# Kernel tuning notes

Hardware: AMD Instinct MI355X
Metric: run time of the kernel (lower is better)

The kernel has to match this reference:

```python
import jax, jax.numpy as jnp
import numpy as np

BATCH = 1048576
INPUT_DIM = 64
DEPTH = 7
N_INTERNAL = 2 ** DEPTH - 1  # 127
N_LEAVES = 2 ** DEPTH        # 128


def setup_inputs() -> dict:
    key = jax.random.key(0)
    kx, kw = jax.random.split(key)
    x = jax.random.normal(kx, (BATCH, INPUT_DIM), dtype=jnp.float32)
    node_weights = jax.random.normal(kw, (N_INTERNAL, INPUT_DIM), dtype=jnp.float32) * 0.01
    node_biases = jnp.zeros((N_INTERNAL,), dtype=jnp.float32)
    leaf_values = jnp.linspace(0.0, 1.0, N_LEAVES, dtype=jnp.float32)
    return {"x": x, "node_weights": node_weights, "node_biases": node_biases,
            "leaf_values": leaf_values}


def _leaf_probs(x, node_weights, node_biases, depth):
    # All node routing probabilities in one GEMM (BFS node order matches idx order).
    logits = jnp.einsum('bd,nd->bn', x, node_weights) + node_biases  # [B, n_internal]
    p_right = jax.nn.sigmoid(logits)
    batch = x.shape[0]
    probs = jnp.ones((batch, 1), dtype=x.dtype)  # root prob
    idx = 0
    for d in range(depth):
        n = 1 << d
        pd = p_right[:, idx:idx + n]  # [B, n] nodes at level d in BFS order
        # child order: left (2*node) then right (2*node+1) -> interleave
        probs = jnp.stack([probs * (1.0 - pd), probs * pd], axis=-1).reshape(batch, 2 * n)
        idx += n
    return probs  # [B, n_leaves]


def reference(x, node_weights, node_biases, leaf_values):
    leaf_probs = _leaf_probs(x, node_weights, node_biases, DEPTH)
    pred = leaf_probs @ leaf_values  # [B]
    return (pred, leaf_probs)
```

## Files before the change

kernel.cpp:

```cpp
#include <hip/hip_runtime.h>


typedef float v4f __attribute__((ext_vector_type(4)));
typedef _Float16 h8 __attribute__((ext_vector_type(8)));
typedef unsigned int u32;
typedef u32 u32x2 __attribute__((ext_vector_type(2)));

constexpr int BATCH = 1 << 20;
constexpr int PSTRIDE = 40;
constexpr int PWAVE = 128 * PSTRIDE;

__device__ __forceinline__ float fast_sigmoid(float z) {
    float e = __builtin_amdgcn_exp2f(z * -1.44269504088896340736f);
    return __builtin_amdgcn_rcpf(1.0f + e);
}

__device__ __forceinline__ u32 pk2(float a, float b) {
    return __builtin_bit_cast(u32, __builtin_amdgcn_cvt_pkrtz(a, b));
}

__device__ __forceinline__ h8 cvt8(v4f lo, v4f hi) {
    union { u32 w[4]; h8 v; } u;
    u.w[0] = pk2(lo.x, lo.y);
    u.w[1] = pk2(lo.z, lo.w);
    u.w[2] = pk2(hi.x, hi.y);
    u.w[3] = pk2(hi.z, hi.w);
    return u.v;
}

__global__ __launch_bounds__(256, 3) void sdt_kernel(
    const float* __restrict__ x,
    const float* __restrict__ w,
    const float* __restrict__ bias,
    const float* __restrict__ leaf,
    float* __restrict__ pred_out,
    float* __restrict__ lp_out)
{
    __shared__ __align__(16) unsigned char smem[4 * PWAVE];

    const int tid  = threadIdx.x;
    const int lane = tid & 63;
    const int wave = tid >> 6;
    const int lc = lane & 15, lq = lane >> 4;
    const int j = lane & 7,   rsub = lane >> 3;

    unsigned char* Pw = smem + wave * PWAVE;

    h8 bfrag[8][2];
#pragma unroll
    for (int ct = 0; ct < 8; ++ct) {
        int node = ct * 16 + lc; if (node > 126) node = 126;
#pragma unroll
        for (int kh = 0; kh < 2; ++kh) {
            const float* src = w + node * 64 + kh * 32 + lq * 8;
            bfrag[ct][kh] = cvt8(*(const v4f*)src, *(const v4f*)(src + 4));
        }
    }
    float bias_v[8];
#pragma unroll
    for (int ct = 0; ct < 8; ++ct) {
        int node = ct * 16 + lc; if (node > 126) node = 126;
        bias_v[ct] = bias[node];
    }
    v4f leafv[4];
#pragma unroll
    for (int s = 0; s < 4; ++s) leafv[s] = *(const v4f*)(leaf + 32 * s + 4 * j);

    const int b2 = (j >> 2) & 1, b3 = (j >> 1) & 1, b4 = j & 1;
    const int wave_row0 = blockIdx.x * 256 + wave * 16;

    const float* xr0 = x + (size_t)(wave_row0 + lc) * 64 + lq * 8;
    v4f xa = *(const v4f*)xr0,        xb = *(const v4f*)(xr0 + 4);
    v4f xc = *(const v4f*)(xr0 + 32), xd = *(const v4f*)(xr0 + 36);

#pragma unroll
    for (int ck = 0; ck < 4; ++ck) {
        const int row0 = wave_row0 + ck * 64;

        h8 a0 = cvt8(xa, xb);
        h8 a1 = cvt8(xc, xd);
        if (ck < 3) {
            const float* xr = xr0 + (ck + 1) * 64 * 64;
            xa = *(const v4f*)xr;        xb = *(const v4f*)(xr + 4);
            xc = *(const v4f*)(xr + 32); xd = *(const v4f*)(xr + 36);
        }

#pragma unroll
        for (int ct = 0; ct < 8; ++ct) {
            v4f acc = {};
            acc = __builtin_amdgcn_mfma_f32_16x16x32_f16(a0, bfrag[ct][0], acc, 0, 0, 0);
            acc = __builtin_amdgcn_mfma_f32_16x16x32_f16(a1, bfrag[ct][1], acc, 0, 0, 0);
            float s0 = fast_sigmoid(acc[0] + bias_v[ct]);
            float s1 = fast_sigmoid(acc[1] + bias_v[ct]);
            float s2 = fast_sigmoid(acc[2] + bias_v[ct]);
            float s3 = fast_sigmoid(acc[3] + bias_v[ct]);
            *(u32x2*)(Pw + (ct * 16 + lc) * PSTRIDE + lq * 8) =
                u32x2{pk2(s0, s1), pk2(s2, s3)};
        }

        asm volatile("s_waitcnt lgkmcnt(0)" ::: "memory");

        auto rd = [&](int node, int row) -> float {
            return (float)*(const _Float16*)(Pw + node * PSTRIDE + row * 2);
        };

        float pa = 0.f, pb = 0.f;
#pragma unroll
        for (int i1 = 0; i1 < 2; ++i1) {
            const int row = rsub + 8 * i1;
            float p0  = rd(0, row);
            float p1a = rd(1, row), p1b = rd(2, row);
            float f01_0 = (1.f - p0) * (1.f - p1a);
            float f01_1 = (1.f - p0) * p1a;
            float f01_2 = p0 * (1.f - p1b);
            float f01_3 = p0 * p1b;
            float acc = 0.f;
            v4f* dst = (v4f*)lp_out + (size_t)(row0 + row) * 32 + j;
#pragma unroll
            for (int seg = 0; seg < 4; ++seg) {
                float f01 = seg == 0 ? f01_0 : seg == 1 ? f01_1 : seg == 2 ? f01_2 : f01_3;
                float pd2 = rd(3 + seg, row);
                float P3 = f01 * (b2 ? pd2 : 1.f - pd2);
                float pd3 = rd(7 + 2 * seg + (j >> 2), row);
                float P4 = P3 * (b3 ? pd3 : 1.f - pd3);
                float pd4 = rd(15 + 4 * seg + (j >> 1), row);
                float P5 = P4 * (b4 ? pd4 : 1.f - pd4);
                const int q = 8 * seg + j;
                float pd5 = rd(31 + q, row);
                float A = P5 * (1.f - pd5), B = P5 * pd5;
                float pl = rd(63 + 2 * q, row), pr = rd(64 + 2 * q, row);
                v4f o = { A * (1.f - pl), A * pl, B * (1.f - pr), B * pr };
                dst[seg * 8] = o;
                acc = fmaf(o.x, leafv[seg].x, acc);
                acc = fmaf(o.y, leafv[seg].y, acc);
                acc = fmaf(o.z, leafv[seg].z, acc);
                acc = fmaf(o.w, leafv[seg].w, acc);
            }
            if (i1 == 0) pa = acc; else pb = acc;
        }

#pragma unroll
        for (int s = 1; s <= 4; s <<= 1) {
            pa += __shfl_xor(pa, s, 64);
            pb += __shfl_xor(pb, s, 64);
        }
        if (j == 0) {
            pred_out[row0 + rsub]     = pa;
            pred_out[row0 + rsub + 8] = pb;
        }
    }
}

extern "C" void kernel_launch(void* const* d_in, const int* in_sizes, int n_in,
                              void* d_out, int out_size, void* d_ws, size_t ws_size,
                              hipStream_t stream) {
    const float* x    = (const float*)d_in[0];
    const float* w    = (const float*)d_in[1];
    const float* bias = (const float*)d_in[2];
    const float* leaf = (const float*)d_in[3];

    float* pred = (float*)d_out;
    float* lp   = (float*)d_out + BATCH;

    sdt_kernel<<<BATCH / 256, 256, 0, stream>>>(x, w, bias, leaf, pred, lp);
}
```

Before: 178.7 us.

## Stage node weights in swizzled LDS and raise occupancy to four blocks

Node weights are no longer kept as per-lane register fragments. They are converted once per block into an XOR-swizzled fp16 tile in shared memory, and the B fragments are read from LDS inside the GEMM loop. This frees registers so launch bounds can target four blocks per CU, which should help hide the latency of the heavy lp_out stores. The branchy left/right selects are replaced with fma using precomputed sign and offset constants. The cost is extra LDS traffic, 16KB more shared memory per block, and a block-wide sync.

```diff
diff --git a/kernel.cpp b/kernel.cpp
--- a/kernel.cpp
+++ b/kernel.cpp
@@ -9,6 +9,8 @@
 constexpr int BATCH = 1 << 20;
 constexpr int PSTRIDE = 40;
 constexpr int PWAVE = 128 * PSTRIDE;
+constexpr int W_BYTES = 128 * 128;
+constexpr int P_OFF = W_BYTES;
 
 __device__ __forceinline__ float fast_sigmoid(float z) {
     float e = __builtin_amdgcn_exp2f(z * -1.44269504088896340736f);
@@ -28,7 +30,7 @@
     return u.v;
 }
 
-__global__ __launch_bounds__(256, 3) void sdt_kernel(
+__global__ __launch_bounds__(256, 4) void sdt_kernel(
     const float* __restrict__ x,
     const float* __restrict__ w,
     const float* __restrict__ bias,
@@ -36,7 +38,7 @@
     float* __restrict__ pred_out,
     float* __restrict__ lp_out)
 {
-    __shared__ __align__(16) unsigned char smem[4 * PWAVE];
+    __shared__ __align__(16) unsigned char smem[W_BYTES + 4 * PWAVE];
 
     const int tid  = threadIdx.x;
     const int lane = tid & 63;
@@ -44,18 +46,20 @@
     const int lc = lane & 15, lq = lane >> 4;
     const int j = lane & 7,   rsub = lane >> 3;
 
-    unsigned char* Pw = smem + wave * PWAVE;
+    unsigned char* WL = smem;
+    unsigned char* Pw = smem + P_OFF + wave * PWAVE;
 
-    h8 bfrag[8][2];
-#pragma unroll
-    for (int ct = 0; ct < 8; ++ct) {
-        int node = ct * 16 + lc; if (node > 126) node = 126;
-#pragma unroll
-        for (int kh = 0; kh < 2; ++kh) {
-            const float* src = w + node * 64 + kh * 32 + lq * 8;
-            bfrag[ct][kh] = cvt8(*(const v4f*)src, *(const v4f*)(src + 4));
+    for (int idx = tid; idx < 128 * 8; idx += 256) {
+        int node = idx >> 3, c = idx & 7;
+        v4f f0 = {}, f1 = {};
+        if (node < 127) {
+            const float* sp = w + node * 64 + c * 8;
+            f0 = *(const v4f*)sp; f1 = *(const v4f*)(sp + 4);
         }
+        int off = node * 128 + ((c * 16) ^ ((node & 7) << 4));
+        *(h8*)(WL + off) = cvt8(f0, f1);
     }
+
     float bias_v[8];
 #pragma unroll
     for (int ct = 0; ct < 8; ++ct) {
@@ -67,11 +71,18 @@
     for (int s = 0; s < 4; ++s) leafv[s] = *(const v4f*)(leaf + 32 * s + 4 * j);
 
     const int b2 = (j >> 2) & 1, b3 = (j >> 1) & 1, b4 = j & 1;
+    const float s2 = b2 ? 1.f : -1.f, o2 = b2 ? 0.f : 1.f;
+    const float s3 = b3 ? 1.f : -1.f, o3 = b3 ? 0.f : 1.f;
+    const float s4 = b4 ? 1.f : -1.f, o4 = b4 ? 0.f : 1.f;
+
     const int wave_row0 = blockIdx.x * 256 + wave * 16;
+    const int wsw = (lc & 7) << 4;
 
     const float* xr0 = x + (size_t)(wave_row0 + lc) * 64 + lq * 8;
     v4f xa = *(const v4f*)xr0,        xb = *(const v4f*)(xr0 + 4);
     v4f xc = *(const v4f*)(xr0 + 32), xd = *(const v4f*)(xr0 + 36);
+
+    __syncthreads();
 
 #pragma unroll
     for (int ck = 0; ck < 4; ++ck) {
@@ -87,15 +98,18 @@
 
 #pragma unroll
         for (int ct = 0; ct < 8; ++ct) {
+            const unsigned char* wrow = WL + (ct * 16 + lc) * 128;
+            h8 b0 = *(const h8*)(wrow + ((lq * 16)      ^ wsw));
+            h8 b1 = *(const h8*)(wrow + ((64 + lq * 16) ^ wsw));
             v4f acc = {};
-            acc = __builtin_amdgcn_mfma_f32_16x16x32_f16(a0, bfrag[ct][0], acc, 0, 0, 0);
-            acc = __builtin_amdgcn_mfma_f32_16x16x32_f16(a1, bfrag[ct][1], acc, 0, 0, 0);
+            acc = __builtin_amdgcn_mfma_f32_16x16x32_f16(a0, b0, acc, 0, 0, 0);
+            acc = __builtin_amdgcn_mfma_f32_16x16x32_f16(a1, b1, acc, 0, 0, 0);
             float s0 = fast_sigmoid(acc[0] + bias_v[ct]);
             float s1 = fast_sigmoid(acc[1] + bias_v[ct]);
-            float s2 = fast_sigmoid(acc[2] + bias_v[ct]);
-            float s3 = fast_sigmoid(acc[3] + bias_v[ct]);
+            float sS2 = fast_sigmoid(acc[2] + bias_v[ct]);
+            float sS3 = fast_sigmoid(acc[3] + bias_v[ct]);
             *(u32x2*)(Pw + (ct * 16 + lc) * PSTRIDE + lq * 8) =
-                u32x2{pk2(s0, s1), pk2(s2, s3)};
+                u32x2{pk2(s0, s1), pk2(sS2, sS3)};
         }
 
         asm volatile("s_waitcnt lgkmcnt(0)" ::: "memory");
@@ -119,12 +133,9 @@
 #pragma unroll
             for (int seg = 0; seg < 4; ++seg) {
                 float f01 = seg == 0 ? f01_0 : seg == 1 ? f01_1 : seg == 2 ? f01_2 : f01_3;
-                float pd2 = rd(3 + seg, row);
-                float P3 = f01 * (b2 ? pd2 : 1.f - pd2);
-                float pd3 = rd(7 + 2 * seg + (j >> 2), row);
-                float P4 = P3 * (b3 ? pd3 : 1.f - pd3);
-                float pd4 = rd(15 + 4 * seg + (j >> 1), row);
-                float P5 = P4 * (b4 ? pd4 : 1.f - pd4);
+                float P3 = f01 * fmaf(s2, rd(3 + seg, row), o2);
+                float P4 = P3  * fmaf(s3, rd(7 + 2 * seg + (j >> 2), row), o3);
+                float P5 = P4  * fmaf(s4, rd(15 + 4 * seg + (j >> 1), row), o4);
                 const int q = 8 * seg + j;
                 float pd5 = rd(31 + q, row);
                 float A = P5 * (1.f - pd5), B = P5 * pd5;
```

Result: faster. 164.0 us (median of 2 runs) (-8.2%).
